# Performance work log

Hardware: AMD Instinct MI355X
Metric: run time of the kernel (lower is better)

The kernel has to match this reference:

```python
import jax, jax.numpy as jnp
import numpy as np

SIGMA = 0.05  # Gaussian CTF width for probe_model(k) = exp(-k^2 / (2*SIGMA^2))
H, W = 2048, 2048
MARGIN = 16
N_POS = 1_000_000


def setup_inputs() -> dict:
    key = jax.random.key(0)
    k1, k2 = jax.random.split(key)
    # positions are (x, y) pairs covering the field of view
    positions = jax.random.uniform(k1, (N_POS, 2), dtype=jnp.float32) * jnp.array([W - 2.0, H - 2.0], jnp.float32)
    intensities = jax.random.uniform(k2, (N_POS,), dtype=jnp.float32) + 0.5
    # |k| grid on the padded canvas, exactly as in __init__
    kx = np.fft.fftfreq(W + 2 * MARGIN)
    ky = np.fft.fftfreq(H + 2 * MARGIN)
    kgrid = jnp.asarray(np.sqrt(kx[None] ** 2 + ky[:, None] ** 2), dtype=jnp.float32)
    return {"positions": positions, "intensities": intensities, "k": kgrid, "margin": MARGIN}


def probe_model(k):
    return jnp.exp(-(k ** 2) / (2.0 * SIGMA ** 2))


def reference(positions, intensities, k, margin):
    Hp, Wp = k.shape  # padded shape = (H+2m, W+2m)
    pos = positions + margin  # (N, 2) as (x, y)
    rounded = jnp.floor(pos).astype(jnp.int32)
    rows = jnp.clip(rounded[:, 1], 0, Hp - 1)
    cols = jnp.clip(rounded[:, 0], 0, Wp - 1)
    dy = pos[:, 1] - rows.astype(pos.dtype)
    dx = pos[:, 0] - cols.astype(pos.dtype)
    rows1 = (rows + 1) % Hp
    cols1 = (cols + 1) % Wp
    # bilinear scatter-add splat (true accumulation for duplicate indices)
    arr = jnp.zeros((Hp, Wp), dtype=pos.dtype)
    arr = arr.at[rows, cols].add((1.0 - dy) * (1.0 - dx) * intensities)
    arr = arr.at[rows1, cols].add(dy * (1.0 - dx) * intensities)
    arr = arr.at[rows, cols1].add((1.0 - dy) * dx * intensities)
    # note: (rows - y) * (cols - x) == dy * dx, matching the torch source
    arr = arr.at[rows1, cols1].add(dy * dx * intensities)
    # FFT-domain multiply by the probe transfer function
    out = jnp.fft.ifftn(jnp.fft.fftn(arr, axes=(-2, -1)) * probe_model(k), axes=(-2, -1)).real
    return out[margin:-margin, margin:-margin]
```

## Files before the change

kernel.cpp:

```cpp
#include <hip/hip_runtime.h>
#include <hip/hip_fp16.h>
#include <math.h>

#define HP   2080
#define WP   2080
#define MARG 16
#define HOUT 2048
#define WOUT 2048
#define RAD  16

#define TGRID 32
#define NBIN  1024
#define CAP   2560

#define NBLK 256
#define THR  1024
#define PPT  4
#define RCAP 10240

#define AST  97
#define INV  0xffffffffu

#define FSCALE    33554432.0f
#define FINVSCALE 2.9802322387695312e-8f

__device__ __forceinline__ void make_weights(float* wreg) {
#pragma unroll
    for (int t = 0; t <= RAD; ++t)
        wreg[t] = 0.12533141373155003f * __expf(-0.04934802200544679f * (float)(t * t));
}

__global__ __launch_bounds__(THR) void scatter_kernel(const float2* __restrict__ pos,
                                                      const float* __restrict__ inten,
                                                      int* __restrict__ cursor,
                                                      ushort4* __restrict__ bins,
                                                      int n) {
    __shared__ int     lhist[NBIN];
    __shared__ int     lofs[NBIN];
    __shared__ int     lbase[NBIN];
    __shared__ int     wsum[16];
    __shared__ int     stot;
    __shared__ ushort4 lrec[RCAP];
    __shared__ ushort  lbin[RCAP];

    const int tid = threadIdx.x;
    lhist[tid] = 0;
    __syncthreads();

    const int stride = NBLK * THR;
    const int start  = blockIdx.x * THR + tid;
    unsigned ra[PPT], rb[PPT], rc[PPT];
    unsigned p0[PPT], p1[PPT], p2[PPT], p3[PPT];

#pragma unroll
    for (int it = 0; it < PPT; ++it) {
        int i = start + it * stride;
        p0[it] = p1[it] = p2[it] = p3[it] = INV;
        ra[it] = 0;
        if (i < n) {
            float2 p = pos[i];
            float I  = inten[i];
            float px = p.x + MARG, py = p.y + MARG;
            int col = (int)floorf(px), row = (int)floorf(py);
            row = min(max(row, 0), HP - 1);
            col = min(max(col, 0), WP - 1);
            float dy = py - (float)row, dx = px - (float)col;
            ra[it] = ((unsigned)row << 12) | (unsigned)col;
            rb[it] = (unsigned)__half_as_ushort(__float2half(dx))
                   | ((unsigned)__half_as_ushort(__float2half(dy)) << 16);
            rc[it] = (unsigned)__half_as_ushort(__float2half(I));
            int tIlo = max(0, ((row + 32) >> 6) - 1), tIhi = min(TGRID - 1, (row + 1) >> 6);
            int tJlo = max(0, ((col + 32) >> 6) - 1), tJhi = min(TGRID - 1, (col + 1) >> 6);
            int b00 = (tIlo << 5) | tJlo;
            p0[it] = ((unsigned)b00 << 16) | (unsigned)atomicAdd(&lhist[b00], 1);
            if (tJhi > tJlo) {
                int b = (tIlo << 5) | tJhi;
                p1[it] = ((unsigned)b << 16) | (unsigned)atomicAdd(&lhist[b], 1);
            }
            if (tIhi > tIlo) {
                int b = (tIhi << 5) | tJlo;
                p2[it] = ((unsigned)b << 16) | (unsigned)atomicAdd(&lhist[b], 1);
                if (tJhi > tJlo) {
                    int b2 = (tIhi << 5) | tJhi;
                    p3[it] = ((unsigned)b2 << 16) | (unsigned)atomicAdd(&lhist[b2], 1);
                }
            }
        }
    }
    __syncthreads();

    int c = lhist[tid];
    int incl = c;
    for (int d = 1; d < 64; d <<= 1) {
        int u = __shfl_up(incl, d, 64);
        if ((tid & 63) >= d) incl += u;
    }
    if ((tid & 63) == 63) wsum[tid >> 6] = incl;
    __syncthreads();
    if (tid == 0) {
        int s = 0;
        for (int w = 0; w < 16; ++w) { int x = wsum[w]; wsum[w] = s; s += x; }
        stot = s;
    }
    __syncthreads();
    lofs[tid]  = incl - c + wsum[tid >> 6];
    lbase[tid] = (c > 0) ? atomicAdd(&cursor[tid], c) : 0;
    __syncthreads();

#pragma unroll
    for (int it = 0; it < PPT; ++it) {
        const int row = (int)(ra[it] >> 12), col = (int)(ra[it] & 4095u);
        ushort4 rec;
        rec.y = (unsigned short)(rb[it] & 0xffffu);
        rec.z = (unsigned short)(rb[it] >> 16);
        rec.w = (unsigned short)rc[it];
        auto place = [&](unsigned pv) {
            if (pv != INV) {
                int bin  = (int)(pv >> 16);
                int rank = (int)(pv & 0xffffu);
                int fr1  = row - ((bin >> 5) << 6) + 1;
                int fc1  = col - ((bin & 31) << 6) + 1;
                int slot = lofs[bin] + rank;
                if (slot < RCAP) {
                    rec.x = (unsigned short)((fr1 << 7) | fc1);
                    lrec[slot] = rec;
                    lbin[slot] = (unsigned short)bin;
                }
            }
        };
        place(p0[it]); place(p1[it]); place(p2[it]); place(p3[it]);
    }
    __syncthreads();

    const int total = min(stot, RCAP);
    for (int j = tid; j < total; j += THR) {
        int b = lbin[j];
        int g = lbase[b] + (j - lofs[b]);
        if (g < CAP) bins[(size_t)b * CAP + g] = lrec[j];
    }
}

__device__ __forceinline__ void splat_rec(ushort4 r, unsigned long long* U) {
    int fr1 = r.x >> 7, fc1 = r.x & 127;
    float dx = __half2float(__ushort_as_half(r.y));
    float dy = __half2float(__ushort_as_half(r.z));
    float I  = __half2float(__ushort_as_half(r.w));
    float wy1 = dy * I, wy0 = I - wy1;
    float wl, wh; int k;
    if (fc1 & 1) { k = fc1 >> 1;        wl = 1.0f - dx; wh = dx; }
    else {         k = 48 + (fc1 >> 1); wl = (fc1 >= 1) ? 1.0f - dx : 0.0f;
                                        wh = (fc1 <= 95) ? dx : 0.0f; }
    if (fr1 >= 1) {
        unsigned long long v = ((unsigned long long)(unsigned)(wy0 * wh * FSCALE) << 32)
                             |  (unsigned long long)(unsigned)(wy0 * wl * FSCALE);
        atomicAdd(&U[(fr1 - 1) * 97 + k], v);
    }
    if (fr1 <= 95) {
        unsigned long long v = ((unsigned long long)(unsigned)(wy1 * wh * FSCALE) << 32)
                             |  (unsigned long long)(unsigned)(wy1 * wl * FSCALE);
        atomicAdd(&U[fr1 * 97 + k], v);
    }
}

__global__ __launch_bounds__(1024) void splat_conv(const ushort4* __restrict__ bins,
                                                   const int* __restrict__ cursor,
                                                   float* __restrict__ out) {
    __shared__ unsigned long long U[96 * 97];
    float* A = (float*)U;
    const int tid = threadIdx.x;
    const int b  = blockIdx.x;
    const int tI = b >> 5, tJ = b & 31;

    const int cnt = min(cursor[b], CAP);
    const ushort4* bp = bins + (size_t)b * CAP;
    const bool h0 = tid < cnt, h1 = tid + 1024 < cnt, h2 = tid + 2048 < cnt;
    ushort4 r0_ = {0,0,0,0}, r1_ = {0,0,0,0}, r2_ = {0,0,0,0};
    if (h0) r0_ = bp[tid];
    if (h1) r1_ = bp[tid + 1024];
    if (h2) r2_ = bp[tid + 2048];

    uint4* U4 = (uint4*)U;
    for (int i = tid; i < 4656; i += 1024) U4[i] = make_uint4(0u, 0u, 0u, 0u);
    __syncthreads();

    if (h0) splat_rec(r0_, U);
    if (h1) splat_rec(r1_, U);
    if (h2) splat_rec(r2_, U);
    __syncthreads();

    float m0a=0,m0b=0,m1a=0,m1b=0,m2a=0,m2b=0,m3a=0,m3b=0,m4a=0,m4b=0;
#define MERGE_READ(K, RA, RB) { int u = tid + (K) * 1024; if (u < 4608) { \
        int r = u / 48, cp = u - r * 48; \
        unsigned long long e  = U[r * 97 + cp]; \
        unsigned long long ol = U[r * 97 + 48 + cp]; \
        unsigned long long orr= U[r * 97 + 48 + cp + 1]; \
        RA = ((float)(unsigned)e         + (float)(unsigned)(ol >> 32)) * FINVSCALE; \
        RB = ((float)(unsigned)(e >> 32) + (float)(unsigned)orr)        * FINVSCALE; } }
    MERGE_READ(0, m0a, m0b)
    MERGE_READ(1, m1a, m1b)
    MERGE_READ(2, m2a, m2b)
    MERGE_READ(3, m3a, m3b)
    MERGE_READ(4, m4a, m4b)
    __syncthreads();
#define MERGE_WRITE(K, RA, RB) { int u = tid + (K) * 1024; if (u < 4608) { \
        int r = u / 48, cp = u - r * 48; \
        A[r * AST + 2 * cp] = RA; A[r * AST + 2 * cp + 1] = RB; } }
    MERGE_WRITE(0, m0a, m0b)
    MERGE_WRITE(1, m1a, m1b)
    MERGE_WRITE(2, m2a, m2b)
    MERGE_WRITE(3, m3a, m3b)
    MERGE_WRITE(4, m4a, m4b)
    __syncthreads();

    float wreg[RAD + 1];
    make_weights(wreg);

    if (tid < 768) {
        const int j = tid >> 3;
        const int o = (tid & 7) << 3;
        float* Ar = &A[j * AST + o];
        float Wf[40];
#pragma unroll
        for (int t = 0; t < 40; ++t) Wf[t] = Ar[t];
        float a[8] = {0, 0, 0, 0, 0, 0, 0, 0};
#pragma unroll
        for (int t = 0; t < 40; ++t) {
            float v = Wf[t];
#pragma unroll
            for (int k = 0; k < 8; ++k)
                if (t >= k && t <= k + 32)
                    a[k] += v * wreg[(t - k - 16 < 0) ? (k + 16 - t) : (t - k - 16)];
        }
#pragma unroll
        for (int k = 0; k < 8; ++k) Ar[k] = a[k];
    }
    __syncthreads();

    const int lx = tid & 63;
    const int y0 = (tid >> 6) << 2;
    float Wf[36];
#pragma unroll
    for (int t = 0; t < 36; ++t) Wf[t] = A[(y0 + t) * AST + lx];
    float a[4] = {0, 0, 0, 0};
#pragma unroll
    for (int t = 0; t < 36; ++t) {
        float v = Wf[t];
#pragma unroll
        for (int k = 0; k < 4; ++k)
            if (t >= k && t <= k + 32)
                a[k] += v * wreg[(t - k - 16 < 0) ? (k + 16 - t) : (t - k - 16)];
    }
    const int orow = (tI << 6) + y0, ocol = (tJ << 6) + lx;
#pragma unroll
    for (int k = 0; k < 4; ++k)
        out[(size_t)(orow + k) * WOUT + ocol] = a[k];
}

extern "C" void kernel_launch(void* const* d_in, const int* in_sizes, int n_in,
                              void* d_out, int out_size, void* d_ws, size_t ws_size,
                              hipStream_t stream) {
    const float2* pos   = (const float2*)d_in[0];
    const float*  inten = (const float*)d_in[1];
    int n = in_sizes[1];

    ushort4* bins   = (ushort4*)d_ws;
    int*     cursor = (int*)((char*)d_ws + (size_t)NBIN * CAP * sizeof(ushort4));

    hipMemsetAsync(cursor, 0, NBIN * sizeof(int), stream);
    scatter_kernel<<<NBLK, THR, 0, stream>>>(pos, inten, cursor, bins, n);
    splat_conv<<<NBIN, 1024, 0, stream>>>(bins, cursor, (float*)d_out);
}
```

Measured before the change: 110.3 us.

## Pack all four bilinear corner weights into one 16-bit-field 64-bit shared atomic

The splat stage now quantizes the four bilinear corner weights to 16-bit fixed point and packs them into a single 64-bit word. That word is added with one shared-memory atomic into one of four parity-indexed accumulation arrays, replacing the previous two 64-bit atomics per record. The merge step reads six packed words per output pair and unpacks their fields. This halves the atomic traffic, but 16-bit fields with a scale of 2048 give coarser precision and can overflow when many points land in the same cell. The global cursor atomic in the scatter kernel is also issued before the prefix scan so its latency can overlap.

```diff
diff --git a/kernel.cpp b/kernel.cpp
--- a/kernel.cpp
+++ b/kernel.cpp
@@ -21,8 +21,14 @@
 #define AST  97
 #define INV  0xffffffffu
 
-#define FSCALE    33554432.0f
-#define FINVSCALE 2.9802322387695312e-8f
+#define IAA 0
+#define IAS 2304
+#define ISA 4656
+#define ISS 7008
+#define QSZ 9412
+
+#define QSCALE 2048.0f
+#define QINV   4.8828125e-4f
 
 __device__ __forceinline__ void make_weights(float* wreg) {
 #pragma unroll
@@ -90,6 +96,8 @@
     __syncthreads();
 
     int c = lhist[tid];
+    int gbase = (c > 0) ? atomicAdd(&cursor[tid], c) : 0;
+
     int incl = c;
     for (int d = 1; d < 64; d <<= 1) {
         int u = __shfl_up(incl, d, 64);
@@ -104,7 +112,7 @@
     }
     __syncthreads();
     lofs[tid]  = incl - c + wsum[tid >> 6];
-    lbase[tid] = (c > 0) ? atomicAdd(&cursor[tid], c) : 0;
+    lbase[tid] = gbase;
     __syncthreads();
 
 #pragma unroll
@@ -140,33 +148,31 @@
     }
 }
 
-__device__ __forceinline__ void splat_rec(ushort4 r, unsigned long long* U) {
+__device__ __forceinline__ void splat_rec(ushort4 r, unsigned long long* Q) {
     int fr1 = r.x >> 7, fc1 = r.x & 127;
     float dx = __half2float(__ushort_as_half(r.y));
     float dy = __half2float(__ushort_as_half(r.z));
     float I  = __half2float(__ushort_as_half(r.w));
     float wy1 = dy * I, wy0 = I - wy1;
-    float wl, wh; int k;
-    if (fc1 & 1) { k = fc1 >> 1;        wl = 1.0f - dx; wh = dx; }
-    else {         k = 48 + (fc1 >> 1); wl = (fc1 >= 1) ? 1.0f - dx : 0.0f;
-                                        wh = (fc1 <= 95) ? dx : 0.0f; }
-    if (fr1 >= 1) {
-        unsigned long long v = ((unsigned long long)(unsigned)(wy0 * wh * FSCALE) << 32)
-                             |  (unsigned long long)(unsigned)(wy0 * wl * FSCALE);
-        atomicAdd(&U[(fr1 - 1) * 97 + k], v);
-    }
-    if (fr1 <= 95) {
-        unsigned long long v = ((unsigned long long)(unsigned)(wy1 * wh * FSCALE) << 32)
-                             |  (unsigned long long)(unsigned)(wy1 * wl * FSCALE);
-        atomicAdd(&U[fr1 * 97 + k], v);
-    }
+    float wx1 = dx, wx0 = 1.0f - dx;
+    unsigned f00 = (unsigned)(wy0 * wx0 * QSCALE + 0.5f);
+    unsigned f01 = (unsigned)(wy0 * wx1 * QSCALE + 0.5f);
+    unsigned f10 = (unsigned)(wy1 * wx0 * QSCALE + 0.5f);
+    unsigned f11 = (unsigned)(wy1 * wx1 * QSCALE + 0.5f);
+    unsigned long long v = (unsigned long long)(f00 | (f01 << 16))
+                         | ((unsigned long long)(f10 | (f11 << 16)) << 32);
+    int R = fr1 >> 1, C = fc1 >> 1;
+    int idx;
+    if (fr1 & 1) idx = (fc1 & 1) ? (IAA + R * 48 + C) : (IAS + R * 49 + C);
+    else         idx = (fc1 & 1) ? (ISA + R * 48 + C) : (ISS + R * 49 + C);
+    atomicAdd(&Q[idx], v);
 }
 
 __global__ __launch_bounds__(1024) void splat_conv(const ushort4* __restrict__ bins,
                                                    const int* __restrict__ cursor,
                                                    float* __restrict__ out) {
-    __shared__ unsigned long long U[96 * 97];
-    float* A = (float*)U;
+    __shared__ unsigned long long Q[QSZ];
+    float* A = (float*)Q;
     const int tid = threadIdx.x;
     const int b  = blockIdx.x;
     const int tI = b >> 5, tJ = b & 31;
@@ -179,23 +185,30 @@
     if (h1) r1_ = bp[tid + 1024];
     if (h2) r2_ = bp[tid + 2048];
 
-    uint4* U4 = (uint4*)U;
-    for (int i = tid; i < 4656; i += 1024) U4[i] = make_uint4(0u, 0u, 0u, 0u);
-    __syncthreads();
-
-    if (h0) splat_rec(r0_, U);
-    if (h1) splat_rec(r1_, U);
-    if (h2) splat_rec(r2_, U);
+    uint4* U4 = (uint4*)Q;
+    for (int i = tid; i < 4706; i += 1024) U4[i] = make_uint4(0u, 0u, 0u, 0u);
+    __syncthreads();
+
+    if (h0) splat_rec(r0_, Q);
+    if (h1) splat_rec(r1_, Q);
+    if (h2) splat_rec(r2_, Q);
     __syncthreads();
 
     float m0a=0,m0b=0,m1a=0,m1b=0,m2a=0,m2b=0,m3a=0,m3b=0,m4a=0,m4b=0;
+#define FLD(q, rs, cs) ((unsigned)((q) >> ((rs) * 32 + (cs) * 16)) & 0xffffu)
 #define MERGE_READ(K, RA, RB) { int u = tid + (K) * 1024; if (u < 4608) { \
-        int r = u / 48, cp = u - r * 48; \
-        unsigned long long e  = U[r * 97 + cp]; \
-        unsigned long long ol = U[r * 97 + 48 + cp]; \
-        unsigned long long orr= U[r * 97 + 48 + cp + 1]; \
-        RA = ((float)(unsigned)e         + (float)(unsigned)(ol >> 32)) * FINVSCALE; \
-        RB = ((float)(unsigned)(e >> 32) + (float)(unsigned)orr)        * FINVSCALE; } }
+        int r = u / 48, p = u - r * 48; \
+        int Rp = r >> 1, rs = r & 1; \
+        int Rs = (r + 1) >> 1, rss = rs ^ 1; \
+        unsigned long long qaa  = Q[IAA + Rp * 48 + p]; \
+        unsigned long long qas0 = Q[IAS + Rp * 49 + p]; \
+        unsigned long long qas1 = Q[IAS + Rp * 49 + p + 1]; \
+        unsigned long long qsa  = Q[ISA + Rs * 48 + p]; \
+        unsigned long long qss0 = Q[ISS + Rs * 49 + p]; \
+        unsigned long long qss1 = Q[ISS + Rs * 49 + p + 1]; \
+        unsigned s0 = FLD(qaa, rs, 0) + FLD(qas0, rs, 1) + FLD(qsa, rss, 0) + FLD(qss0, rss, 1); \
+        unsigned s1 = FLD(qaa, rs, 1) + FLD(qas1, rs, 0) + FLD(qsa, rss, 1) + FLD(qss1, rss, 0); \
+        RA = (float)s0 * QINV; RB = (float)s1 * QINV; } }
     MERGE_READ(0, m0a, m0b)
     MERGE_READ(1, m1a, m1b)
     MERGE_READ(2, m2a, m2b)
@@ -203,8 +216,8 @@
     MERGE_READ(4, m4a, m4b)
     __syncthreads();
 #define MERGE_WRITE(K, RA, RB) { int u = tid + (K) * 1024; if (u < 4608) { \
-        int r = u / 48, cp = u - r * 48; \
-        A[r * AST + 2 * cp] = RA; A[r * AST + 2 * cp + 1] = RB; } }
+        int r = u / 48, p = u - r * 48; \
+        A[r * AST + 2 * p] = RA; A[r * AST + 2 * p + 1] = RB; } }
     MERGE_WRITE(0, m0a, m0b)
     MERGE_WRITE(1, m1a, m1b)
     MERGE_WRITE(2, m2a, m2b)
```

After: 117.7 us. +6.8%, slower.
